# Performance work log

Measured on AMD Instinct MI355X. Metric: run time of the kernel, lower is better.

Reference implementation:

```python
import jax, jax.numpy as jnp
import numpy as np

IN_F, OUT_F, GROUP = 4096, 4096, 128
N_GROUPS = IN_F // GROUP  # 32


def setup_inputs() -> dict:
    key = jax.random.key(0)
    k1, k2, k3, k4, k5 = jax.random.split(key, 5)
    x = jax.random.normal(k1, (2, 1024, IN_F), dtype=jnp.float32)
    w_q = jax.random.randint(k2, (OUT_F, N_GROUPS, GROUP), -128, 128, dtype=jnp.int32)  # int8-range quantized weights
    s_w = jax.random.uniform(k3, (N_GROUPS, OUT_F), dtype=jnp.float32) * 0.01  # per-group, per-out-channel scales
    perm = jax.random.permutation(k4, IN_F).astype(jnp.int64)  # GPTQ activation-order permutation
    bias = jax.random.normal(k5, (OUT_F,), dtype=jnp.float32)
    return {"x": x, "w_q": w_q, "s_w": s_w, "perm": perm, "bias": bias}


def reference(x, w_q, s_w, perm, bias):
    prefix = x.shape[:-1]
    orig_dtype = x.dtype
    xf = x.reshape(-1, IN_F)          # (n, in)
    xf = xf[:, perm]                  # apply GPTQ permutation
    xf = xf.reshape(-1, N_GROUPS, GROUP).astype(jnp.float32)  # (n, g, k)
    wf = w_q.astype(jnp.float32)      # (o, g, k) dequant-to-fp32 weights (pre-scale)
    y_g = jnp.einsum('ngk,ogk->ngo', xf, wf)   # per-group partial products (n, g, o)
    y = jnp.sum(y_g * s_w[None, :, :], axis=1) # apply group scales, reduce groups -> (n, o)
    y = y + bias.astype(y.dtype)
    return y.reshape(*prefix, OUT_F).astype(orig_dtype)
```

## Files before the change

### kernel.cpp

```cpp
#include <hip/hip_runtime.h>
#include <hip/hip_bf16.h>
#include <stdint.h>

#define IN_F   4096
#define OUT_F  4096
#define M_ROWS 2048
#define NG     32
#define GRP    128

typedef __bf16 bf16x8 __attribute__((ext_vector_type(8)));
typedef float  f32x4  __attribute__((ext_vector_type(4)));

typedef const void __attribute__((address_space(1))) cv_g;
typedef void       __attribute__((address_space(3))) v_l;

__device__ __forceinline__ void async16(const void* g, void* l) {
  __builtin_amdgcn_global_load_lds((cv_g*)g, (v_l*)l, 16, 0, 0);
}

__device__ int g_perm_is64;

__global__ void decode_flag(const void* __restrict__ perm_raw) {
  if (threadIdx.x == 0 && blockIdx.x == 0) {
    const int* w = (const int*)perm_raw;
    int ok = 1;
    for (int j = 0; j < 32; ++j) {
      int lo = w[2 * j], hi = w[2 * j + 1];
      if (hi != 0 || lo < 0 || lo >= IN_F) { ok = 0; break; }
    }
    g_perm_is64 = ok;
  }
}

__global__ __launch_bounds__(256) void prep(const float* __restrict__ x,
                                            const int* __restrict__ w_q,
                                            const float* __restrict__ s_w,
                                            const void* __restrict__ perm_raw,
                                            __hip_bfloat16* __restrict__ xp,
                                            __hip_bfloat16* __restrict__ wf) {
  __shared__ float sx[IN_F];
  __shared__ int sflag;
  const int b = blockIdx.x;
  const int t = threadIdx.x;

  if (b < M_ROWS) {
    const int m = b;
    const float* xr = x + (size_t)m * IN_F;
#pragma unroll
    for (int u = 0; u < 4; ++u) {
      int idx = (u * 256 + t) * 4;
      *(float4*)&sx[idx] = *(const float4*)&xr[idx];
    }
    if (t < 64) {
      const int* w = (const int*)perm_raw;
      int j = t & 31;
      int lo = w[2 * j], hi = w[2 * j + 1];
      int cond = (hi == 0 && lo >= 0 && lo < IN_F);
      unsigned long long bal = __ballot(cond);
      if (t == 0) sflag = (bal == ~0ull) ? 1 : 0;
    }
    __syncthreads();
    const int f = sflag;
    const long long* p64 = (const long long*)perm_raw;
    const int*       p32 = (const int*)perm_raw;
    const int jb = t * 16;
    __hip_bfloat16 tmp[16] __attribute__((aligned(16)));
#pragma unroll
    for (int u = 0; u < 16; ++u) {
      int pj = f ? (int)p64[jb + u] : p32[jb + u];
      tmp[u] = __float2bfloat16(sx[pj]);
    }
    *(uint4*)(xp + (size_t)m * IN_F + jb)     = *(const uint4*)&tmp[0];
    *(uint4*)(xp + (size_t)m * IN_F + jb + 8) = *(const uint4*)&tmp[8];
  } else {
    int tt = (b - M_ROWS) * 256 + t;
    int o  = tt >> 9;
    int kb = (tt & 511) << 3;
    float s = s_w[(size_t)(kb >> 7) * OUT_F + o];
    const int* wr = w_q + (size_t)o * IN_F + kb;
    int4 w0 = *(const int4*)wr;
    int4 w1 = *(const int4*)(wr + 4);
    __hip_bfloat16 tmp[8] __attribute__((aligned(16)));
    tmp[0] = __float2bfloat16((float)w0.x * s);
    tmp[1] = __float2bfloat16((float)w0.y * s);
    tmp[2] = __float2bfloat16((float)w0.z * s);
    tmp[3] = __float2bfloat16((float)w0.w * s);
    tmp[4] = __float2bfloat16((float)w1.x * s);
    tmp[5] = __float2bfloat16((float)w1.y * s);
    tmp[6] = __float2bfloat16((float)w1.z * s);
    tmp[7] = __float2bfloat16((float)w1.w * s);
    *(uint4*)(wf + (size_t)o * IN_F + kb) = *(const uint4*)tmp;
  }
}

__global__ __launch_bounds__(256) void gemm_bt(
    const __hip_bfloat16* __restrict__ A,
    const __hip_bfloat16* __restrict__ B,
    const float* __restrict__ bias,
    float* __restrict__ C) {
  __shared__ __hip_bfloat16 smem[2][16384];

  const int tid  = threadIdx.x;
  const int wave = tid >> 6;
  const int lane = tid & 63;
  const int bm = blockIdx.y << 7;
  const int bn = blockIdx.x << 7;
  const int wm = (wave >> 1) << 6;
  const int wn = (wave & 1) << 6;
  const int lrow = lane & 15;
  const int quad = lane >> 4;

  f32x4 acc[4][4] = {};

  const __hip_bfloat16* gA[4];
  const __hip_bfloat16* gB[4];
  int lbase[4];
#pragma unroll
  for (int h = 0; h < 4; ++h) {
    int L   = h * 256 + wave * 64 + lane;
    int row = L >> 3;
    int kc  = (L & 7) ^ (row & 7);
    gA[h] = A + (size_t)(bm + row) * IN_F + kc * 8;
    gB[h] = B + (size_t)(bn + row) * IN_F + kc * 8;
    lbase[h] = (h * 256 + wave * 64) * 8;
  }

  auto stage = [&](__hip_bfloat16* buf, int kn) {
#pragma unroll
    for (int h = 0; h < 4; ++h) {
      async16(gA[h] + kn, buf + lbase[h]);
      async16(gB[h] + kn, buf + 8192 + lbase[h]);
    }
  };

  auto compute = [&](const __hip_bfloat16* buf) {
#pragma unroll
    for (int s = 0; s < 2; ++s) {
      const int kcp = ((s << 2) + quad) ^ (lrow & 7);
      bf16x8 af[4], bfr[4];
#pragma unroll
      for (int i = 0; i < 4; ++i)
        af[i] = *(const bf16x8*)&buf[(wm + i * 16 + lrow) * 64 + kcp * 8];
#pragma unroll
      for (int j = 0; j < 4; ++j)
        bfr[j] = *(const bf16x8*)&buf[8192 + (wn + j * 16 + lrow) * 64 + kcp * 8];
#pragma unroll
      for (int i = 0; i < 4; ++i)
#pragma unroll
        for (int j = 0; j < 4; ++j)
          acc[i][j] = __builtin_amdgcn_mfma_f32_16x16x32_bf16(af[i], bfr[j], acc[i][j], 0, 0, 0);
    }
  };

  stage(smem[0], 0);
  for (int k0 = 0; k0 < IN_F; k0 += 128) {
    __syncthreads();
    stage(smem[1], k0 + 64);
    compute(smem[0]);
    __syncthreads();
    if (k0 + 128 < IN_F) stage(smem[0], k0 + 128);
    compute(smem[1]);
  }

#pragma unroll
  for (int i = 0; i < 4; ++i) {
    int row = bm + wm + i * 16 + quad * 4;
#pragma unroll
    for (int j = 0; j < 4; ++j) {
      int col = bn + wn + j * 16 + lrow;
      float bv = bias[col];
#pragma unroll
      for (int r = 0; r < 4; ++r)
        C[(size_t)(row + r) * OUT_F + col] = acc[i][j][r] + bv;
    }
  }
}

__global__ void naive_fallback(const float* __restrict__ x, const int* __restrict__ w_q,
                               const float* __restrict__ s_w, const void* __restrict__ perm_raw,
                               const float* __restrict__ bias, float* __restrict__ out) {
  int t = blockIdx.x * blockDim.x + threadIdx.x;
  int m = t >> 12;
  int o = t & 4095;
  const int f = g_perm_is64;
  const long long* p64 = (const long long*)perm_raw;
  const int*       p32 = (const int*)perm_raw;
  const float* xr = x + (size_t)m * IN_F;
  const int*   wr = w_q + (size_t)o * IN_F;
  float acc = 0.f;
  for (int g = 0; g < NG; ++g) {
    float part = 0.f;
    for (int k = 0; k < GRP; ++k) {
      int j = g * GRP + k;
      int pj = f ? (int)p64[j] : p32[j];
      part += xr[pj] * (float)wr[j];
    }
    acc += part * s_w[(size_t)g * OUT_F + o];
  }
  out[t] = acc + bias[o];
}

extern "C" void kernel_launch(void* const* d_in, const int* in_sizes, int n_in,
                              void* d_out, int out_size, void* d_ws, size_t ws_size,
                              hipStream_t stream) {
  const float* x    = (const float*)d_in[0];
  const int*   w_q  = (const int*)d_in[1];
  const float* s_w  = (const float*)d_in[2];
  const void*  perm = d_in[3];
  const float* bias = (const float*)d_in[4];
  float* out = (float*)d_out;

  const size_t xp_bytes = (size_t)M_ROWS * IN_F * sizeof(__hip_bfloat16);
  const size_t wf_bytes = (size_t)OUT_F * IN_F * sizeof(__hip_bfloat16);

  if (ws_size < xp_bytes + wf_bytes) {
    decode_flag<<<1, 64, 0, stream>>>(perm);
    naive_fallback<<<(M_ROWS * OUT_F) / 256, 256, 0, stream>>>(x, w_q, s_w, perm, bias, out);
    return;
  }

  __hip_bfloat16* xp = (__hip_bfloat16*)d_ws;
  __hip_bfloat16* wf = (__hip_bfloat16*)((char*)d_ws + xp_bytes);

  prep<<<M_ROWS + (OUT_F * IN_F / 8) / 256, 256, 0, stream>>>(x, w_q, s_w, perm, xp, wf);

  dim3 grid(OUT_F / 128, M_ROWS / 128);
  gemm_bt<<<grid, 256, 0, stream>>>(xp, wf, bias, out);
}
```

Before: 215.6 us.

## Enlarge GEMM tile to 128x256 with 8 waves and intra-block split-K

The bf16 GEMM now uses 512-thread blocks covering a 128x256 output tile. Each wave computes a 64x128 sub-tile over half of every 64-wide K chunk, and the two K halves are summed through shared memory at the end. The larger tile improves operand reuse from LDS and halves the number of blocks. In exchange it needs 96KB of LDS per block, 128 accumulator floats per thread, and a serialized reduction epilogue, all of which can limit occupancy.

```diff
diff --git a/kernel.cpp b/kernel.cpp
--- a/kernel.cpp
+++ b/kernel.cpp
@@ -93,85 +93,109 @@
   }
 }
 
-__global__ __launch_bounds__(256) void gemm_bt(
+__global__ __launch_bounds__(512, 2) void gemm_bt(
     const __hip_bfloat16* __restrict__ A,
     const __hip_bfloat16* __restrict__ B,
     const float* __restrict__ bias,
     float* __restrict__ C) {
-  __shared__ __hip_bfloat16 smem[2][16384];
+  __shared__ __hip_bfloat16 smem[49152];
 
   const int tid  = threadIdx.x;
-  const int wave = tid >> 6;
+  const int w    = tid >> 6;
   const int lane = tid & 63;
+  const int wr   = w >> 2;
+  const int wc   = (w >> 1) & 1;
+  const int kv   = w & 1;
   const int bm = blockIdx.y << 7;
-  const int bn = blockIdx.x << 7;
-  const int wm = (wave >> 1) << 6;
-  const int wn = (wave & 1) << 6;
+  const int bn = blockIdx.x << 8;
   const int lrow = lane & 15;
   const int quad = lane >> 4;
 
-  f32x4 acc[4][4] = {};
-
-  const __hip_bfloat16* gA[4];
-  const __hip_bfloat16* gB[4];
-  int lbase[4];
-#pragma unroll
-  for (int h = 0; h < 4; ++h) {
-    int L   = h * 256 + wave * 64 + lane;
-    int row = L >> 3;
-    int kc  = (L & 7) ^ (row & 7);
-    gA[h] = A + (size_t)(bm + row) * IN_F + kc * 8;
-    gB[h] = B + (size_t)(bn + row) * IN_F + kc * 8;
-    lbase[h] = (h * 256 + wave * 64) * 8;
-  }
-
-  auto stage = [&](__hip_bfloat16* buf, int kn) {
-#pragma unroll
-    for (int h = 0; h < 4; ++h) {
-      async16(gA[h] + kn, buf + lbase[h]);
-      async16(gB[h] + kn, buf + 8192 + lbase[h]);
-    }
+  f32x4 acc[4][8] = {};
+
+  const __hip_bfloat16* gp[6];
+  int lbase[6];
+#pragma unroll
+  for (int h = 0; h < 6; ++h) {
+    int c = h * 512 + w * 64 + lane;
+    if (c < 1024) {
+      int row = c >> 3;
+      int kc  = (c & 7) ^ (row & 7);
+      gp[h] = A + (size_t)(bm + row) * IN_F + kc * 8;
+      lbase[h] = (h * 512 + w * 64) * 8;
+    } else {
+      int cb  = c - 1024;
+      int row = cb >> 3;
+      int kc  = (cb & 7) ^ (row & 7);
+      gp[h] = B + (size_t)(bn + row) * IN_F + kc * 8;
+      lbase[h] = 8192 + ((h - 2) * 512 + w * 64) * 8;
+    }
+  }
+
+  auto stage = [&](int bufofs, int kn) {
+#pragma unroll
+    for (int h = 0; h < 6; ++h)
+      async16(gp[h] + kn, &smem[bufofs + lbase[h]]);
   };
 
-  auto compute = [&](const __hip_bfloat16* buf) {
-#pragma unroll
-    for (int s = 0; s < 2; ++s) {
-      const int kcp = ((s << 2) + quad) ^ (lrow & 7);
-      bf16x8 af[4], bfr[4];
+  const int kc_log = (kv << 2) + quad;
+  auto compute = [&](int bufofs) {
+    bf16x8 af[4];
+#pragma unroll
+    for (int i = 0; i < 4; ++i) {
+      int row = (wr << 6) + i * 16 + lrow;
+      af[i] = *(const bf16x8*)&smem[bufofs + row * 64 + (kc_log ^ (row & 7)) * 8];
+    }
+#pragma unroll
+    for (int j = 0; j < 8; ++j) {
+      int rowb = (wc << 7) + j * 16 + lrow;
+      bf16x8 bfr = *(const bf16x8*)&smem[bufofs + 8192 + rowb * 64 + (kc_log ^ (rowb & 7)) * 8];
 #pragma unroll
       for (int i = 0; i < 4; ++i)
-        af[i] = *(const bf16x8*)&buf[(wm + i * 16 + lrow) * 64 + kcp * 8];
-#pragma unroll
-      for (int j = 0; j < 4; ++j)
-        bfr[j] = *(const bf16x8*)&buf[8192 + (wn + j * 16 + lrow) * 64 + kcp * 8];
+        acc[i][j] = __builtin_amdgcn_mfma_f32_16x16x32_bf16(af[i], bfr, acc[i][j], 0, 0, 0);
+    }
+  };
+
+  stage(0, 0);
+  for (int k0 = 0; k0 < IN_F; k0 += 128) {
+    __syncthreads();
+    stage(24576, k0 + 64);
+    compute(0);
+    __syncthreads();
+    if (k0 + 128 < IN_F) stage(0, k0 + 128);
+    compute(24576);
+  }
+
+  float* red = (float*)&smem[0];
+#pragma unroll
+  for (int t = 0; t < 2; ++t) {
+    __syncthreads();
+    if (wr == t && kv == 1) {
+      float* dst = red + wc * 8192;
 #pragma unroll
       for (int i = 0; i < 4; ++i)
 #pragma unroll
-        for (int j = 0; j < 4; ++j)
-          acc[i][j] = __builtin_amdgcn_mfma_f32_16x16x32_bf16(af[i], bfr[j], acc[i][j], 0, 0, 0);
-    }
-  };
-
-  stage(smem[0], 0);
-  for (int k0 = 0; k0 < IN_F; k0 += 128) {
-    __syncthreads();
-    stage(smem[1], k0 + 64);
-    compute(smem[0]);
-    __syncthreads();
-    if (k0 + 128 < IN_F) stage(smem[0], k0 + 128);
-    compute(smem[1]);
-  }
-
-#pragma unroll
-  for (int i = 0; i < 4; ++i) {
-    int row = bm + wm + i * 16 + quad * 4;
-#pragma unroll
-    for (int j = 0; j < 4; ++j) {
-      int col = bn + wn + j * 16 + lrow;
-      float bv = bias[col];
-#pragma unroll
-      for (int r = 0; r < 4; ++r)
-        C[(size_t)(row + r) * OUT_F + col] = acc[i][j][r] + bv;
+        for (int j = 0; j < 8; ++j)
+#pragma unroll
+          for (int r = 0; r < 4; ++r)
+            dst[(i * 16 + quad * 4 + r) * 128 + j * 16 + lrow] = acc[i][j][r];
+    }
+    __syncthreads();
+    if (wr == t && kv == 0) {
+      const float* src = red + wc * 8192;
+#pragma unroll
+      for (int i = 0; i < 4; ++i) {
+        int row = bm + (wr << 6) + i * 16 + quad * 4;
+#pragma unroll
+        for (int j = 0; j < 8; ++j) {
+          int col = bn + (wc << 7) + j * 16 + lrow;
+          float bv = bias[col];
+#pragma unroll
+          for (int r = 0; r < 4; ++r)
+            C[(size_t)(row + r) * OUT_F + col] =
+                acc[i][j][r] + src[(i * 16 + quad * 4 + r) * 128 + j * 16 + lrow] + bv;
+        }
+      }
     }
   }
 }
@@ -224,6 +248,6 @@
 
   prep<<<M_ROWS + (OUT_F * IN_F / 8) / 256, 256, 0, stream>>>(x, w_q, s_w, perm, xp, wf);
 
-  dim3 grid(OUT_F / 128, M_ROWS / 128);
-  gemm_bt<<<grid, 256, 0, stream>>>(xp, wf, bias, out);
-}
+  dim3 grid(OUT_F / 256, M_ROWS / 128);
+  gemm_bt<<<grid, 512, 0, stream>>>(xp, wf, bias, out);
+}
```

Measured after the change: 219.4 us. Within noise of the previous version (+1.8%).
